# Kernel tuning notes

Hardware: AMD Instinct MI355X
Metric: run time of the kernel (lower is better)

The kernel has to match this reference:

```python
import jax, jax.numpy as jnp
import numpy as np

B, D, F, P = 65536, 256, 512, 256


def setup_inputs() -> dict:
    key = jax.random.key(0)
    k_x, k_f, k_p, k_a, k_b, k_t = jax.random.split(key, 6)
    x = jax.random.normal(k_x, (B, D), dtype=jnp.float32)
    # reset_parameters: uniform(-0.27, 1)
    features = jax.random.uniform(k_f, (F, D), dtype=jnp.float32, minval=-0.27, maxval=1.0)
    prototypes = jax.random.uniform(k_p, (P, D), dtype=jnp.float32, minval=-0.27, maxval=1.0)
    # alpha/beta/theta init to zeros in the module; use small random values so the
    # output is non-trivial for kernel correctness checking.
    alpha = jax.random.normal(k_a, (1,), dtype=jnp.float32) * 0.1
    beta = jax.random.normal(k_b, (1,), dtype=jnp.float32) * 0.1
    theta = jax.random.normal(k_t, (1,), dtype=jnp.float32) * 0.1
    return {"x": x, "features": features, "prototypes": prototypes,
            "alpha": alpha, "beta": beta, "theta": theta}


def reference(x, features, prototypes, alpha, beta, theta):
    # Shared projections
    x_features = x @ features.T                 # [B, F]
    p_features = prototypes @ features.T        # [P, F]
    x_present = jax.nn.relu(x_features)         # [B, F]
    p_present = jax.nn.relu(p_features)         # [P, F]
    x_weighted = x_features * x_present         # [B, F]
    p_weighted = p_features * p_present         # [P, F]

    # Tversky terms
    common = x_weighted @ p_weighted.T                          # [B, P]
    x_weighted_sum = jnp.sum(x_weighted, axis=1, keepdims=True)  # [B, 1]
    x_p_interaction = x_weighted @ p_present.T                  # [B, P]
    x_distinctive = x_weighted_sum - x_p_interaction            # [B, P]
    p_weighted_sum = jnp.sum(p_weighted, axis=1)[None, :]        # [1, P]
    x_p_weighted_interaction = x_present @ p_weighted.T         # [B, P]
    p_distinctive = p_weighted_sum - x_p_weighted_interaction   # [B, P]

    return theta * common - alpha * x_distinctive - beta * p_distinctive
```

## Files before the change

### kernel.cpp

```cpp
#include <hip/hip_runtime.h>
#include <cstdint>
#include <cstddef>

#define Bsz 65536
#define Dsz 256
#define Fsz 512
#define Psz 256

typedef __attribute__((ext_vector_type(8))) short short8;
typedef __attribute__((ext_vector_type(4))) short short4v;
typedef __attribute__((ext_vector_type(4))) float float4v;
typedef __attribute__((ext_vector_type(16))) float float16v;
typedef __attribute__((ext_vector_type(4))) unsigned uint4v;

__device__ inline short f2bf(float f) {
    unsigned u = __builtin_bit_cast(unsigned, f);
    u = (u + 0x7FFFu + ((u >> 16) & 1u)) >> 16;
    return (short)u;
}
__device__ inline float bf2f(short s) {
    unsigned u = ((unsigned)(unsigned short)s) << 16;
    return __builtin_bit_cast(float, u);
}
__device__ inline unsigned cvt_pk_bf16(float lo, float hi) {
    unsigned r;
    asm("v_cvt_pk_bf16_f32 %0, %1, %2" : "=v"(r) : "v"(lo), "v"(hi));
    return r;
}


#define SBPITCH 136

__global__ __launch_bounds__(256, 2) void k_pre(
    const float* __restrict__ prototypes, const float* __restrict__ features,
    const float* __restrict__ alpha_p, const float* __restrict__ beta_p,
    const float* __restrict__ theta_p,
    short* __restrict__ featbB, short* __restrict__ pab, float* __restrict__ pws_part)
{
    __shared__ char lds[65536 + 17408];
    short* FB = (short*)lds;
    short* As = (short*)(lds + 65536);
    short* Sb = (short*)(lds + 65536);

    const int t = threadIdx.x;
    const int w = t >> 6, lane = t & 63, l15 = lane & 15, l4 = lane >> 4;
    const int rowg = blockIdx.x >> 2, nc = blockIdx.x & 3;
    const float alpha = *alpha_p, beta = *beta_p, theta = *theta_p;

    #pragma unroll
    for (int it = 0; it < 16; ++it) {
        int u = it * 256 + t;
        int ftl = u >> 10, dtl = (u >> 6) & 15, ln = u & 63;
        const float* src = features + (size_t)(nc * 128 + ftl * 32 + (ln & 31)) * Dsz
                         + dtl * 16 + (ln >> 5) * 8;
        float4v v0 = *(const float4v*)src;
        float4v v1 = *(const float4v*)(src + 4);
        uint4v uv;
        uv.x = cvt_pk_bf16(v0.x, v0.y);
        uv.y = cvt_pk_bf16(v0.z, v0.w);
        uv.z = cvt_pk_bf16(v1.x, v1.y);
        uv.w = cvt_pk_bf16(v1.z, v1.w);
        short8 sv = __builtin_bit_cast(short8, uv);
        *(short8*)&FB[u * 8] = sv;
        if (rowg == 0) {
            int go = (((nc * 4 + ftl) * 16 + dtl) * 64 + ln) * 8;
            *(short8*)&featbB[go] = sv;
        }
    }

    float4v acc[2][4];
    #pragma unroll
    for (int a = 0; a < 2; ++a)
        #pragma unroll
        for (int b = 0; b < 4; ++b) acc[a][b] = (float4v){0.f, 0.f, 0.f, 0.f};

    const float* pbase = prototypes + (size_t)rowg * 64 * Dsz;

    for (int kc = 0; kc < 4; ++kc) {
        __syncthreads();
        #pragma unroll
        for (int j = 0; j < 4; ++j) {
            int idx = j * 1024 + t * 4;
            int r = idx >> 6, c = idx & 63;
            float4v v = *(const float4v*)(pbase + (size_t)r * Dsz + kc * 64 + c);
            int unit = r * 8 + ((c >> 3) ^ (r & 7));
            short4v s4; s4.x = f2bf(v.x); s4.y = f2bf(v.y); s4.z = f2bf(v.z); s4.w = f2bf(v.w);
            *(short4v*)((char*)As + unit * 16 + (c & 7) * 2) = s4;
        }
        __syncthreads();
        #pragma unroll
        for (int kk = 0; kk < 2; ++kk) {
            short8 af[2], bfr[4];
            const int k8 = kk * 4 + l4;
            #pragma unroll
            for (int tm = 0; tm < 2; ++tm) {
                int m = (w & 1) * 32 + tm * 16 + l15;
                af[tm] = *(const short8*)&As[(m * 8 + (k8 ^ (m & 7))) * 8];
            }
            #pragma unroll
            for (int tn = 0; tn < 4; ++tn) {
                int fl = ((w >> 1) * 4 + tn) * 16 + l15;
                int dtl = kc * 4 + kk * 2 + (l4 >> 1);
                int lnp = (fl & 31) + 32 * (l4 & 1);
                bfr[tn] = *(const short8*)&FB[(((fl >> 5) * 16 + dtl) * 64 + lnp) * 8];
            }
            #pragma unroll
            for (int tm = 0; tm < 2; ++tm)
                #pragma unroll
                for (int tn = 0; tn < 4; ++tn)
                    acc[tm][tn] = __builtin_amdgcn_mfma_f32_16x16x32_bf16(af[tm], bfr[tn], acc[tm][tn], 0, 0, 0);
        }
    }
    __syncthreads();
    #pragma unroll
    for (int tm = 0; tm < 2; ++tm)
        #pragma unroll
        for (int tn = 0; tn < 4; ++tn)
            #pragma unroll
            for (int r = 0; r < 4; ++r) {
                int row = (w & 1) * 32 + tm * 16 + l4 * 4 + r;
                int col = (w >> 1) * 64 + tn * 16 + l15;
                Sb[row * SBPITCH + col] = f2bf(acc[tm][tn][r]);
            }
    __syncthreads();
    #pragma unroll
    for (int rep = 0; rep < 4; ++rep) {
        int u = rep * 256 + t;
        int row = u >> 4, i = u & 15;
        short8 sv = *(const short8*)&Sb[row * SBPITCH + i * 8];
        uint4v u0, u1;
        float sum = 0.f;
        #pragma unroll
        for (int e = 0; e < 8; ++e) {
            float pf = bf2f(sv[e]);
            float pp = fmaxf(pf, 0.f);
            float pw = pf * pp;
            float a0 = theta * pw + alpha * (pp - 1.f);
            float b0 = beta * pw;
            sum += pw;
            unsigned pk = cvt_pk_bf16(a0, b0);
            if (e < 4) u0[e] = pk; else u1[e - 4] = pk;
        }
        int p = rowg * 64 + row;
        int c = 4 * nc + (i >> 2), s2 = i & 3, pt = p >> 5;
        int base = ((c * 4 + s2) * 8 + pt) * 512;
        *(short8*)&pab[base + (p & 31) * 8] = __builtin_bit_cast(short8, u0);
        *(short8*)&pab[base + ((p & 31) + 32) * 8] = __builtin_bit_cast(short8, u1);
        #pragma unroll
        for (int mk = 1; mk < 16; mk <<= 1) sum += __shfl_xor(sum, mk, 64);
        if (l15 == 0) pws_part[nc * 256 + p] = -beta * sum;
    }
}

__global__ __launch_bounds__(256, 2) void k_main(
    const float* __restrict__ x, const short* __restrict__ featbB,
    const short* __restrict__ pab, const float* __restrict__ pws_part,
    float* __restrict__ out)
{
    __shared__ short XL[16384];

    const int t = threadIdx.x;
    const int w = t >> 6, lane = t & 63, l31 = lane & 31, h = lane >> 5;
    const size_t row0 = (size_t)blockIdx.x * 64;

    #pragma unroll
    for (int it = 0; it < 8; ++it) {
        int idx = it * 256 + t;
        int mt_i = idx >> 10, dt_i = (idx >> 6) & 15, ln = idx & 63;
        const float* src = x + (row0 + mt_i * 32 + (ln & 31)) * Dsz + dt_i * 16 + (ln >> 5) * 8;
        float4v v0 = *(const float4v*)src;
        float4v v1 = *(const float4v*)(src + 4);
        uint4v uv;
        uv.x = cvt_pk_bf16(v0.x, v0.y);
        uv.y = cvt_pk_bf16(v0.z, v0.w);
        uv.z = cvt_pk_bf16(v1.x, v1.y);
        uv.w = cvt_pk_bf16(v1.z, v1.w);
        *(short8*)&XL[idx * 8] = __builtin_bit_cast(short8, uv);
    }
    __syncthreads();

    const int mt = w & 1, pth = w >> 1;
    int xoff = mt * 8192 + lane * 8;
    const int a1off = lane * 8;
    const int pboff = (pth * 4) * 512 + lane * 8;

    float16v acc[4];
    #pragma unroll
    for (int a = 0; a < 4; ++a)
        #pragma unroll
        for (int e = 0; e < 16; ++e) acc[a][e] = 0.f;

    short8 A1[16];
    short8 PB[16];
    #pragma unroll
    for (int dt = 0; dt < 16; ++dt)
        A1[dt] = *(const short8*)(featbB + a1off + dt * 512);
    #pragma unroll
    for (int ptl = 0; ptl < 4; ++ptl)
        #pragma unroll
        for (int s = 0; s < 4; ++s)
            PB[ptl * 4 + s] = *(const short8*)(pab + pboff + s * 4096 + ptl * 512);

    #pragma unroll 1
    for (int c = 0; c < 16; ++c) {
        asm volatile("" : "+v"(xoff));

        float16v C1;
        #pragma unroll
        for (int e = 0; e < 16; ++e) C1[e] = 0.f;
        #pragma unroll
        for (int dt = 0; dt < 16; ++dt) {
            short8 xfr = *(const short8*)&XL[xoff + dt * 512];
            C1 = __builtin_amdgcn_mfma_f32_32x32x16_bf16(A1[dt], xfr, C1, 0, 0, 0);
        }

        {
            const short* a1n = featbB + ((c + 1) & 15) * 8192 + a1off;
            #pragma unroll
            for (int dt = 0; dt < 16; ++dt)
                A1[dt] = *(const short8*)(a1n + dt * 512);
        }

        short8 A2f[4];
        #pragma unroll
        for (int s = 0; s < 4; ++s) {
            uint4v uf;
            #pragma unroll
            for (int q = 0; q < 4; ++q) {
                float xf = C1[4 * s + q];
                float xp = fmaxf(xf, 0.f);
                float xw = xf * xp;
                uf[q] = cvt_pk_bf16(xw, xp);
            }
            A2f[s] = __builtin_bit_cast(short8, uf);
        }

        #pragma unroll
        for (int s = 0; s < 4; ++s)
            #pragma unroll
            for (int ptl = 0; ptl < 4; ++ptl)
                acc[ptl] = __builtin_amdgcn_mfma_f32_32x32x16_bf16(A2f[s], PB[ptl * 4 + s], acc[ptl], 0, 0, 0);

        {
            const short* pbn = pab + ((c + 1) & 15) * 16384 + pboff;
            #pragma unroll
            for (int ptl = 0; ptl < 4; ++ptl)
                #pragma unroll
                for (int s = 0; s < 4; ++s)
                    PB[ptl * 4 + s] = *(const short8*)(pbn + s * 4096 + ptl * 512);
        }
    }

    #pragma unroll
    for (int ptl = 0; ptl < 4; ++ptl) {
        int pcol = (pth * 4 + ptl) * 32 + l31;
        float pn = pws_part[pcol] + pws_part[256 + pcol] + pws_part[512 + pcol] + pws_part[768 + pcol];
        #pragma unroll
        for (int r = 0; r < 16; ++r) {
            size_t m = row0 + mt * 32 + (r & 3) + 8 * (r >> 2) + 4 * h;
            out[m * Psz + pcol] = acc[ptl][r] + pn;
        }
    }
}

extern "C" void kernel_launch(void* const* d_in, const int* in_sizes, int n_in,
                              void* d_out, int out_size, void* d_ws, size_t ws_size,
                              hipStream_t stream) {
    const float* x          = (const float*)d_in[0];
    const float* features   = (const float*)d_in[1];
    const float* prototypes = (const float*)d_in[2];
    const float* alpha      = (const float*)d_in[3];
    const float* beta       = (const float*)d_in[4];
    const float* theta      = (const float*)d_in[5];
    float* out = (float*)d_out;

    char* ws = (char*)d_ws;
    short* featbB   = (short*)(ws);
    short* pab      = (short*)(ws + 262144);
    float* pws_part = (float*)(ws + 786432);

    hipLaunchKernelGGL(k_pre,  dim3(16),   dim3(256), 0, stream,
                       prototypes, features, alpha, beta, theta, featbB, pab, pws_part);
    hipLaunchKernelGGL(k_main, dim3(1024), dim3(256), 0, stream,
                       x, featbB, pab, pws_part, out);
}
```

Before: 195.8 us.

## Stage feature tiles in double-buffered LDS via async global-to-LDS loads

Replaces per-wave register loads of the feature matrix tile with cooperative global_load_lds transfers into a double-buffered LDS area, so the four waves share one copy and the next chunk is prefetched while the current one is used. Half of the x fragments are cached in registers, and MFMA groups are wrapped in s_setprio to favour matrix issue. This lowers redundant global traffic and register pressure but adds a per-iteration block barrier and more LDS use, which may affect occupancy.

```diff
diff --git a/kernel.cpp b/kernel.cpp
--- a/kernel.cpp
+++ b/kernel.cpp
@@ -26,6 +26,11 @@
     unsigned r;
     asm("v_cvt_pk_bf16_f32 %0, %1, %2" : "=v"(r) : "v"(lo), "v"(hi));
     return r;
+}
+__device__ inline void gl_lds16(const short* g, short* lds) {
+    __builtin_amdgcn_global_load_lds((const __attribute__((address_space(1))) unsigned*)g,
+                                     (__attribute__((address_space(3))) unsigned*)lds,
+                                     16, 0, 0);
 }
 
 
@@ -158,6 +163,7 @@
     float* __restrict__ out)
 {
     __shared__ short XL[16384];
+    __shared__ short FBL[16384];
 
     const int t = threadIdx.x;
     const int w = t >> 6, lane = t & 63, l31 = lane & 31, h = lane >> 5;
@@ -177,12 +183,23 @@
         uv.w = cvt_pk_bf16(v1.z, v1.w);
         *(short8*)&XL[idx * 8] = __builtin_bit_cast(short8, uv);
     }
+
+    #pragma unroll
+    for (int i = 0; i < 4; ++i) {
+        int dt = w * 4 + i;
+        gl_lds16(featbB + dt * 512 + lane * 8, &FBL[dt * 512]);
+    }
     __syncthreads();
 
     const int mt = w & 1, pth = w >> 1;
-    int xoff = mt * 8192 + lane * 8;
-    const int a1off = lane * 8;
-    const int pboff = (pth * 4) * 512 + lane * 8;
+    int xbase = mt * 8192 + lane * 8;
+    const int lane8 = lane * 8;
+    const int pboff = (pth * 4) * 512 + lane8;
+
+    short8 xlo[8];
+    #pragma unroll
+    for (int dt = 0; dt < 8; ++dt)
+        xlo[dt] = *(const short8*)&XL[xbase + dt * 512];
 
     float16v acc[4];
     #pragma unroll
@@ -190,11 +207,7 @@
         #pragma unroll
         for (int e = 0; e < 16; ++e) acc[a][e] = 0.f;
 
-    short8 A1[16];
     short8 PB[16];
-    #pragma unroll
-    for (int dt = 0; dt < 16; ++dt)
-        A1[dt] = *(const short8*)(featbB + a1off + dt * 512);
     #pragma unroll
     for (int ptl = 0; ptl < 4; ++ptl)
         #pragma unroll
@@ -203,25 +216,41 @@
 
     #pragma unroll 1
     for (int c = 0; c < 16; ++c) {
-        asm volatile("" : "+v"(xoff));
+        const int buf = (c & 1) * 8192;
+        const int cn = (c + 1) & 15;
+
+        if (c) __syncthreads();
+        asm volatile("" : "+v"(xbase));
+
+        {
+            const short* gsrc = featbB + (size_t)cn * 8192 + lane8;
+            short* ldst = &FBL[buf ^ 8192];
+            #pragma unroll
+            for (int i = 0; i < 4; ++i) {
+                int dt = w * 4 + i;
+                gl_lds16(gsrc + dt * 512, ldst + dt * 512);
+            }
+        }
 
         float16v C1;
         #pragma unroll
         for (int e = 0; e < 16; ++e) C1[e] = 0.f;
         #pragma unroll
-        for (int dt = 0; dt < 16; ++dt) {
-            short8 xfr = *(const short8*)&XL[xoff + dt * 512];
-            C1 = __builtin_amdgcn_mfma_f32_32x32x16_bf16(A1[dt], xfr, C1, 0, 0, 0);
-        }
-
-        {
-            const short* a1n = featbB + ((c + 1) & 15) * 8192 + a1off;
-            #pragma unroll
-            for (int dt = 0; dt < 16; ++dt)
-                A1[dt] = *(const short8*)(a1n + dt * 512);
-        }
-
-        short8 A2f[4];
+        for (int g = 0; g < 4; ++g) {
+            short8 fbf[4];
+            #pragma unroll
+            for (int i = 0; i < 4; ++i)
+                fbf[i] = *(const short8*)&FBL[buf + (g * 4 + i) * 512 + lane8];
+            __builtin_amdgcn_s_setprio(1);
+            #pragma unroll
+            for (int i = 0; i < 4; ++i) {
+                const int dt = g * 4 + i;
+                short8 xf = (dt < 8) ? xlo[dt] : *(const short8*)&XL[xbase + dt * 512];
+                C1 = __builtin_amdgcn_mfma_f32_32x32x16_bf16(fbf[i], xf, C1, 0, 0, 0);
+            }
+            __builtin_amdgcn_s_setprio(0);
+        }
+
         #pragma unroll
         for (int s = 0; s < 4; ++s) {
             uint4v uf;
@@ -229,20 +258,18 @@
             for (int q = 0; q < 4; ++q) {
                 float xf = C1[4 * s + q];
                 float xp = fmaxf(xf, 0.f);
-                float xw = xf * xp;
-                uf[q] = cvt_pk_bf16(xw, xp);
-            }
-            A2f[s] = __builtin_bit_cast(short8, uf);
-        }
-
-        #pragma unroll
-        for (int s = 0; s < 4; ++s)
+                uf[q] = cvt_pk_bf16(xf * xp, xp);
+            }
+            short8 A2f = __builtin_bit_cast(short8, uf);
+            __builtin_amdgcn_s_setprio(1);
             #pragma unroll
             for (int ptl = 0; ptl < 4; ++ptl)
-                acc[ptl] = __builtin_amdgcn_mfma_f32_32x32x16_bf16(A2f[s], PB[ptl * 4 + s], acc[ptl], 0, 0, 0);
+                acc[ptl] = __builtin_amdgcn_mfma_f32_32x32x16_bf16(A2f, PB[ptl * 4 + s], acc[ptl], 0, 0, 0);
+            __builtin_amdgcn_s_setprio(0);
+        }
 
         {
-            const short* pbn = pab + ((c + 1) & 15) * 16384 + pboff;
+            const short* pbn = pab + (size_t)cn * 16384 + pboff;
             #pragma unroll
             for (int ptl = 0; ptl < 4; ++ptl)
                 #pragma unroll
```

New measurement: 192.7 us. No clear change (-1.6%).
